# Kernel optimization log

Measured on AMD Instinct MI355X. Metric: run time of the kernel, lower is better.

Reference implementation:

```python
import jax, jax.numpy as jnp
import numpy as np

N = 12000      # nodes
E = 384000     # edges (avg degree 32)
IN, HID, OUT = 128, 128, 40
BETA, ITERS = 0.5, 25   # Bjorck order-2 projection params (module defaults)


def setup_inputs() -> dict:
    key = jax.random.key(0)
    ks = jax.random.split(key, 6)
    x = jax.random.normal(ks[0], (N, IN), jnp.float32)
    edge_index = jax.random.randint(ks[1], (2, E), 0, N, dtype=jnp.int32)
    W1 = jax.random.normal(ks[2], (HID, IN), jnp.float32)
    W2 = jax.random.normal(ks[3], (HID, HID), jnp.float32)
    lin_w = jax.random.normal(ks[4], (OUT, HID), jnp.float32) / np.float32(np.sqrt(HID))
    lin_b = jax.random.normal(ks[5], (OUT,), jnp.float32) * 0.01
    return {"x": x, "W1": W1, "W2": W2, "lin_w": lin_w, "lin_b": lin_b,
            "edge_index": edge_index}


def _bjorck(w):
    # order-2 Bjorck orthonormalization (beta fixed at 0.5):
    # w <- 15/8 w - 5/4 w(w^T w) + 3/8 w(w^T w)^2
    for _ in range(ITERS):
        wtw = w.T @ w
        w = 1.875 * w - 1.25 * (w @ wtw) + 0.375 * (w @ (wtw @ wtw))
    return w


def _orthonormal(W):
    # scale_values: sqrt(||W||_inf * ||W||_1) upper-bounds the spectral norm
    # (computed on .data in torch -> stop_gradient here)
    scaling = jnp.sqrt(jnp.abs(W).sum(axis=1).max() * jnp.abs(W).sum(axis=0).max())
    scaling = jax.lax.stop_gradient(scaling)
    return _bjorck(W.T / scaling).T  # [out, in]


def _normalized_adj(edge_index):
    # to_dense_adj (scatter-add) then D^{-1/2} A^T D^{-1/2} exactly as
    # normalize_tensor_adj: adj.dot(D^{-1/2}).T.dot(D^{-1/2})
    r, c = edge_index[0], edge_index[1]
    adj = jnp.zeros((N, N), jnp.float32).at[r, c].add(1.0)
    rowsum = adj.sum(axis=1)
    d = jnp.where(rowsum > 0, rowsum ** -0.5, 0.0)
    return d[:, None] * adj.T * d[None, :]


def reference(x, W1, W2, lin_w, lin_b, edge_index):
    norm_adj = _normalized_adj(edge_index)          # [N, N]
    h = jax.nn.relu(norm_adj @ (x @ _orthonormal(W1).T))   # [N, HID]
    h = jax.nn.relu(norm_adj @ (h @ _orthonormal(W2).T))   # [N, HID]
    # dropout inactive (eval mode)
    logits = h @ lin_w.T + lin_b                    # [N, OUT]
    return jax.nn.log_softmax(logits, axis=1)
```

## Files before the change

### kernel.cpp

```cpp
#include <hip/hip_runtime.h>
#include <math.h>

#define NN 12000
#define EE 384000
#define FF 128
#define NOUT 40
#define BJ_MAX 25
#define NWARM 8
#define EXIT_TOL 3e-3f
#define GEMM_BLOCKS ((NN + 63) / 64)
#define SEG1 3
#define SEG2 6
#define SEG3 9

typedef __attribute__((ext_vector_type(8))) short bf16x8;
typedef __attribute__((ext_vector_type(4))) short s16x4;
typedef __attribute__((ext_vector_type(4))) float f32x4;
typedef unsigned short ushort_t;

__device__ __forceinline__ ushort_t f2bf(float x) {
  unsigned u = __float_as_uint(x);
  unsigned r = (u + 0x7FFFu + ((u >> 16) & 1u)) >> 16;
  return (ushort_t)r;
}
__device__ __forceinline__ float bf2f(ushort_t h) {
  return __uint_as_float(((unsigned)h) << 16);
}
__device__ __forceinline__ int swz(int r, int c) {
  return ((r << 8) + (c << 1)) ^ ((r & 7) << 4);
}

__device__ __forceinline__ void mm_product(const char* Xh, const char* Xl,
    const char* Yh, const char* Yl, int R0, int C0, int lane, f32x4 (&acc)[2][4]) {
  int rl = lane & 15;
  int kq = (lane >> 4) * 8;
  #pragma unroll
  for (int k0 = 0; k0 < 128; k0 += 32) {
    bf16x8 ah[2], al[2];
    #pragma unroll
    for (int i = 0; i < 2; i++) {
      ah[i] = *(const bf16x8*)(Xh + swz(R0 + i * 16 + rl, k0 + kq));
      al[i] = *(const bf16x8*)(Xl + swz(R0 + i * 16 + rl, k0 + kq));
    }
    #pragma unroll
    for (int j = 0; j < 4; j++) {
      bf16x8 bh = *(const bf16x8*)(Yh + swz(C0 + j * 16 + rl, k0 + kq));
      bf16x8 bl = *(const bf16x8*)(Yl + swz(C0 + j * 16 + rl, k0 + kq));
      #pragma unroll
      for (int i = 0; i < 2; i++) {
        acc[i][j] = __builtin_amdgcn_mfma_f32_16x16x32_bf16(ah[i], bh, acc[i][j], 0, 0, 0);
        acc[i][j] = __builtin_amdgcn_mfma_f32_16x16x32_bf16(ah[i], bl, acc[i][j], 0, 0, 0);
        acc[i][j] = __builtin_amdgcn_mfma_f32_16x16x32_bf16(al[i], bh, acc[i][j], 0, 0, 0);
      }
    }
  }
}

__device__ __forceinline__ void store_C(char* Ch, char* Cl, int R0, int C0,
    int lane, f32x4 (&acc)[2][4]) {
  int cl = lane & 15, rq = (lane >> 4) * 4;
  #pragma unroll
  for (int i = 0; i < 2; i++)
  #pragma unroll
  for (int j = 0; j < 4; j++) {
    int col = C0 + j * 16 + cl;
    int row = R0 + i * 16 + rq;
    s16x4 hv, lv;
    #pragma unroll
    for (int t = 0; t < 4; t++) {
      float x = acc[i][j][t];
      ushort_t h = f2bf(x);
      ushort_t lo = f2bf(x - bf2f(h));
      hv[t] = (short)h; lv[t] = (short)lo;
    }
    *(s16x4*)(Ch + swz(col, row)) = hv;
    *(s16x4*)(Cl + swz(col, row)) = lv;
  }
}

__device__ __forceinline__ void store_CR(char* Ch, char* Cl, char* Rh, char* Rl,
    int R0, int C0, int lane, f32x4 (&acc)[2][4]) {
  int cl = lane & 15, rq = (lane >> 4) * 4;
  #pragma unroll
  for (int i = 0; i < 2; i++)
  #pragma unroll
  for (int j = 0; j < 4; j++) {
    int col = C0 + j * 16 + cl;
    int row = R0 + i * 16 + rq;
    s16x4 hv, lv;
    #pragma unroll
    for (int t = 0; t < 4; t++) {
      float x = acc[i][j][t];
      ushort_t h = f2bf(x);
      ushort_t lo = f2bf(x - bf2f(h));
      hv[t] = (short)h; lv[t] = (short)lo;
    }
    *(s16x4*)(Ch + swz(col, row)) = hv;
    *(s16x4*)(Cl + swz(col, row)) = lv;
    #pragma unroll
    for (int t = 0; t < 4; t++) {
      *(ushort_t*)(Rh + swz(row + t, col)) = (ushort_t)(unsigned short)hv[t];
      *(ushort_t*)(Rl + swz(row + t, col)) = (ushort_t)(unsigned short)lv[t];
    }
  }
}

__device__ void bjorck_segment(int L, int s_it, int e_it, int is_last,
    const float* __restrict__ W1, const float* __restrict__ W2,
    ushort_t* __restrict__ wfc, char* __restrict__ state) {
  __shared__ char lds[131072];
  __shared__ float wmax[8];
  char* P0h = lds;
  char* P0l = lds + 32768;
  char* P1h = lds + 65536;
  char* P1l = lds + 98304;
  const float* Wsrc = (L == 0) ? W1 : W2;
  int tid = threadIdx.x;
  int lane = tid & 63;
  int wv = tid >> 6;
  int R0 = (wv >> 1) * 32;
  int C0 = (wv & 1) * 64;
  char* st = state + L * 131072;

  if (s_it == 0) {
    float* f = (float*)lds;
    if (tid < 256) {
      float s = 0.0f;
      if (tid < 128) {
        for (int j = 0; j < FF; j++) s += fabsf(Wsrc[tid * FF + j]);
      } else {
        int c = tid - 128;
        for (int j = 0; j < FF; j++) s += fabsf(Wsrc[j * FF + c]);
      }
      f[tid] = s;
    }
    __syncthreads();
    if (tid == 0) {
      float rm = 0.0f, cm = 0.0f;
      for (int i = 0; i < 128; i++) { rm = fmaxf(rm, f[i]); cm = fmaxf(cm, f[128 + i]); }
      f[256] = 1.0f / sqrtf(rm * cm);
    }
    __syncthreads();
    float inv_s = f[256];
    __syncthreads();
    int r = tid >> 2, c0 = (tid & 3) * 32;
    #pragma unroll
    for (int mm = 0; mm < 32; mm += 8) {
      bf16x8 hv, lv;
      #pragma unroll
      for (int t = 0; t < 8; t++) {
        float x = Wsrc[r * FF + c0 + mm + t] * inv_s;
        ushort_t h = f2bf(x);
        ushort_t lo = f2bf(x - bf2f(h));
        hv[t] = (short)h; lv[t] = (short)lo;
      }
      *(bf16x8*)(P0h + swz(r, c0 + mm)) = hv;
      *(bf16x8*)(P0l + swz(r, c0 + mm)) = lv;
      #pragma unroll
      for (int t = 0; t < 8; t++) {
        *(ushort_t*)(P1h + swz(c0 + mm + t, r)) = (ushort_t)(unsigned short)hv[t];
        *(ushort_t*)(P1l + swz(c0 + mm + t, r)) = (ushort_t)(unsigned short)lv[t];
      }
    }
    __syncthreads();
  } else {
    int4* dst = (int4*)lds;
    const int4* src = (const int4*)st;
    for (int i = tid; i < 8192; i += 512) dst[i] = src[i];
    __syncthreads();
  }

  int done = 0;
  for (int it = s_it; it < e_it; it++) {
    float ca, cb, cc;
    if (it < NWARM)       { ca = 3.4445f; cb = -4.7750f; cc = 2.0315f; }
    else if (it == NWARM) { ca = 2.1479f; cb = -1.7258f; cc = 0.5645f; }
    else                  { ca = 1.875f;  cb = -1.25f;   cc = 0.375f; }

    f32x4 m_acc[2][4] = {};
    mm_product(P0h, P0l, P0h, P0l, R0, C0, lane, m_acc);

    if (it > NWARM) {
      int cl = lane & 15, rq = (lane >> 4) * 4;
      float lmax = 0.0f;
      #pragma unroll
      for (int i = 0; i < 2; i++)
      #pragma unroll
      for (int j = 0; j < 4; j++)
      #pragma unroll
      for (int t = 0; t < 4; t++) {
        int row = R0 + i * 16 + rq + t;
        int col = C0 + j * 16 + cl;
        float d = m_acc[i][j][t] - ((row == col) ? 1.0f : 0.0f);
        lmax = fmaxf(lmax, fabsf(d));
      }
      #pragma unroll
      for (int off = 32; off; off >>= 1) lmax = fmaxf(lmax, __shfl_xor(lmax, off));
      if (lane == 0) wmax[wv] = lmax;
      __syncthreads();
      float gmax = 0.0f;
      #pragma unroll
      for (int w = 0; w < 8; w++) gmax = fmaxf(gmax, wmax[w]);
      if (gmax < EXIT_TOL) { done = 1; break; }
    } else {
      __syncthreads();
    }
    store_C(P0h, P0l, R0, C0, lane, m_acc);
    __syncthreads();

    f32x4 p_acc[2][4] = {};
    mm_product(P0h, P0l, P0h, P0l, R0, C0, lane, p_acc);
    {
      int cl = lane & 15, rq = (lane >> 4) * 4;
      #pragma unroll
      for (int i = 0; i < 2; i++)
      #pragma unroll
      for (int j = 0; j < 4; j++)
      #pragma unroll
      for (int t = 0; t < 4; t++) {
        int row = R0 + i * 16 + rq + t;
        int col = C0 + j * 16 + cl;
        float pv = cb * m_acc[i][j][t] + cc * p_acc[i][j][t];
        if (row == col) pv += ca;
        p_acc[i][j][t] = pv;
      }
    }
    __syncthreads();
    store_C(P0h, P0l, R0, C0, lane, p_acc);
    __syncthreads();

    f32x4 v_acc[2][4] = {};
    mm_product(P0h, P0l, P1h, P1l, R0, C0, lane, v_acc);
    __syncthreads();
    store_CR(P1h, P1l, P0h, P0l, R0, C0, lane, v_acc);
    __syncthreads();
  }

  if (done || is_last) {
    ushort_t* oh = wfc + L * 32768;
    ushort_t* ol = oh + 16384;
    int r = tid >> 2;
    int q = tid & 3;
    #pragma unroll
    for (int b = 0; b < 4; b++) {
      int c0 = q * 32 + b * 8;
      bf16x8 hv = *(const bf16x8*)(P0h + swz(r, c0));
      bf16x8 lv = *(const bf16x8*)(P0l + swz(r, c0));
      *(bf16x8*)(oh + r * FF + c0) = hv;
      *(bf16x8*)(ol + r * FF + c0) = lv;
    }
  } else {
    const int4* src = (const int4*)lds;
    int4* dst = (int4*)st;
    for (int i = tid; i < 8192; i += 512) dst[i] = src[i];
  }
}

__device__ void scan512(const int* __restrict__ cnt, int* __restrict__ rowstart,
    const float* __restrict__ degf, float* __restrict__ dinv) {
  __shared__ int sums[512];
  int tid = threadIdx.x;
  const int CH = 24;
  int base = tid * CH;
  int local[CH];
  int s = 0;
  #pragma unroll
  for (int m = 0; m < CH; m++) {
    int idx = base + m;
    int v = (idx < NN) ? cnt[idx] : 0;
    local[m] = s;
    s += v;
  }
  sums[tid] = s;
  __syncthreads();
  for (int off = 1; off < 512; off <<= 1) {
    int v = (tid >= off) ? sums[tid - off] : 0;
    __syncthreads();
    sums[tid] += v;
    __syncthreads();
  }
  int excl = (tid > 0) ? sums[tid - 1] : 0;
  #pragma unroll
  for (int m = 0; m < CH; m++) {
    int idx = base + m;
    if (idx < NN) rowstart[idx] = excl + local[m];
  }
  if (tid == 511) rowstart[NN] = sums[511];
  for (int i = tid; i < NN; i += 512) {
    float dv = degf[i];
    dinv[i] = (dv > 0.0f) ? (1.0f / sqrtf(dv)) : 0.0f;
  }
}

__global__ __launch_bounds__(512) void k1_seg_deg(const int* __restrict__ ei,
    float* __restrict__ degf, int* __restrict__ cnt,
    const float* __restrict__ W1, const float* __restrict__ W2,
    ushort_t* __restrict__ wfc, char* __restrict__ state) {
  if (blockIdx.x >= 2) {
    int e = (blockIdx.x - 2) * 512 + threadIdx.x;
    if (e < EE) {
      atomicAdd(&degf[ei[e]], 1.0f);
      atomicAdd(&cnt[ei[EE + e]], 1);
    }
    return;
  }
  bjorck_segment(blockIdx.x, 0, SEG1, 0, W1, W2, wfc, state);
}

__global__ __launch_bounds__(512) void k2_seg_scan(const int* __restrict__ cnt,
    int* __restrict__ rowstart, const float* __restrict__ degf, float* __restrict__ dinv,
    const float* __restrict__ W1, const float* __restrict__ W2,
    ushort_t* __restrict__ wfc, char* __restrict__ state) {
  if (blockIdx.x == 2) { scan512(cnt, rowstart, degf, dinv); return; }
  bjorck_segment(blockIdx.x, SEG1, SEG2, 0, W1, W2, wfc, state);
}

__global__ __launch_bounds__(512) void k3_seg_scatter(const int* __restrict__ ei,
    const int* __restrict__ rowstart, int* __restrict__ fill, int* __restrict__ srcl,
    const float* __restrict__ W1, const float* __restrict__ W2,
    ushort_t* __restrict__ wfc, char* __restrict__ state) {
  if (blockIdx.x >= 2) {
    int e = (blockIdx.x - 2) * 512 + threadIdx.x;
    if (e < EE) {
      int r = ei[e], c = ei[EE + e];
      int pos = rowstart[c] + atomicAdd(&fill[c], 1);
      srcl[pos] = r;
    }
    return;
  }
  bjorck_segment(blockIdx.x, SEG2, SEG3, 0, W1, W2, wfc, state);
}

__global__ __launch_bounds__(512) void k4_seg_spmm(const float* __restrict__ X,
    float* __restrict__ Sout, const float* __restrict__ dinv,
    const int* __restrict__ rowstart, const int* __restrict__ srcl,
    const float* __restrict__ W1, const float* __restrict__ W2,
    ushort_t* __restrict__ wfc, char* __restrict__ state) {
  if (blockIdx.x >= 2) {
    int g = threadIdx.x >> 5, lane32 = threadIdx.x & 31;
    int row = (blockIdx.x - 2) * 16 + g;
    int s = rowstart[row], e = rowstart[row + 1];
    const float4* G4 = (const float4*)X;
    float4 a0 = make_float4(0.f, 0.f, 0.f, 0.f);
    float4 a1 = make_float4(0.f, 0.f, 0.f, 0.f);
    int p = s;
    for (; p + 2 <= e; p += 2) {
      int r0 = srcl[p], r1 = srcl[p + 1];
      float d0 = dinv[r0], d1 = dinv[r1];
      float4 g0 = G4[r0 * 32 + lane32];
      float4 g1 = G4[r1 * 32 + lane32];
      a0.x += d0 * g0.x; a0.y += d0 * g0.y; a0.z += d0 * g0.z; a0.w += d0 * g0.w;
      a1.x += d1 * g1.x; a1.y += d1 * g1.y; a1.z += d1 * g1.z; a1.w += d1 * g1.w;
    }
    if (p < e) {
      int r0 = srcl[p];
      float d0 = dinv[r0];
      float4 g0 = G4[r0 * 32 + lane32];
      a0.x += d0 * g0.x; a0.y += d0 * g0.y; a0.z += d0 * g0.z; a0.w += d0 * g0.w;
    }
    float dc = dinv[row];
    float4 o;
    o.x = dc * (a0.x + a1.x); o.y = dc * (a0.y + a1.y);
    o.z = dc * (a0.z + a1.z); o.w = dc * (a0.w + a1.w);
    ((float4*)Sout)[row * 32 + lane32] = o;
    return;
  }
  bjorck_segment(blockIdx.x, SEG3, BJ_MAX, 1, W1, W2, wfc, state);
}

__global__ __launch_bounds__(256) void gemm_mfma(const float* __restrict__ X,
    const ushort_t* __restrict__ wc, float* __restrict__ Out, int do_relu) {
  __shared__ char xlds[32768];
  char* Xh = xlds;
  char* Xl = xlds + 16384;
  int tid = threadIdx.x;
  int row0 = blockIdx.x * 64;

  {
    int r = tid >> 2;
    int q = (tid & 3) * 32;
    int gr = row0 + r;
    #pragma unroll
    for (int b = 0; b < 32; b += 8) {
      bf16x8 hv, lv;
      if (gr < NN) {
        const float4* xp4 = (const float4*)(X + gr * FF + q + b);
        float4 v0 = xp4[0];
        float4 v1 = xp4[1];
        float xv[8] = {v0.x, v0.y, v0.z, v0.w, v1.x, v1.y, v1.z, v1.w};
        #pragma unroll
        for (int t = 0; t < 8; t++) {
          ushort_t h = f2bf(xv[t]);
          hv[t] = (short)h;
          lv[t] = (short)f2bf(xv[t] - bf2f(h));
        }
      } else {
        #pragma unroll
        for (int t = 0; t < 8; t++) { hv[t] = 0; lv[t] = 0; }
      }
      *(bf16x8*)(Xh + swz(r, q + b)) = hv;
      *(bf16x8*)(Xl + swz(r, q + b)) = lv;
    }
  }
  __syncthreads();

  int lane = tid & 63, wv = tid >> 6;
  int R0 = (wv & 1) * 32;
  int C0 = (wv >> 1) * 64;
  int rl = lane & 15, kq = (lane >> 4) * 8;
  f32x4 acc[2][4] = {};
  #pragma unroll
  for (int k0 = 0; k0 < 128; k0 += 32) {
    bf16x8 ah[2], al[2];
    #pragma unroll
    for (int i = 0; i < 2; i++) {
      ah[i] = *(const bf16x8*)(Xh + swz(R0 + i * 16 + rl, k0 + kq));
      al[i] = *(const bf16x8*)(Xl + swz(R0 + i * 16 + rl, k0 + kq));
    }
    #pragma unroll
    for (int j = 0; j < 4; j++) {
      const ushort_t* bp = wc + (C0 + j * 16 + rl) * FF + k0 + kq;
      bf16x8 bh = *(const bf16x8*)bp;
      bf16x8 bl = *(const bf16x8*)(bp + 16384);
      #pragma unroll
      for (int i = 0; i < 2; i++) {
        acc[i][j] = __builtin_amdgcn_mfma_f32_16x16x32_bf16(ah[i], bh, acc[i][j], 0, 0, 0);
        acc[i][j] = __builtin_amdgcn_mfma_f32_16x16x32_bf16(ah[i], bl, acc[i][j], 0, 0, 0);
        acc[i][j] = __builtin_amdgcn_mfma_f32_16x16x32_bf16(al[i], bh, acc[i][j], 0, 0, 0);
      }
    }
  }
  int rq = (lane >> 4) * 4;
  #pragma unroll
  for (int i = 0; i < 2; i++)
  #pragma unroll
  for (int j = 0; j < 4; j++) {
    int col = C0 + j * 16 + rl;
    #pragma unroll
    for (int t = 0; t < 4; t++) {
      int node = row0 + R0 + i * 16 + rq + t;
      float v = acc[i][j][t];
      if (do_relu) v = fmaxf(v, 0.0f);
      if (node < NN) Out[node * FF + col] = v;
    }
  }
}

__global__ __launch_bounds__(256) void spmm_head(const float* __restrict__ G,
    const float* __restrict__ dinv, const int* __restrict__ rowstart,
    const int* __restrict__ srcl, const float* __restrict__ lw,
    const float* __restrict__ lb, float* __restrict__ out) {
  __shared__ float slw[NOUT * 130];
  __shared__ float slb[64];
  __shared__ float sh[8][128];
  int tid = threadIdx.x;
  for (int i = tid; i < NOUT * 32; i += 256) {
    int r = i >> 5, c4 = i & 31;
    float4 v = ((const float4*)lw)[r * 32 + c4];
    float* dst = slw + r * 130 + c4 * 4;
    dst[0] = v.x; dst[1] = v.y; dst[2] = v.z; dst[3] = v.w;
  }
  if (tid < 64) slb[tid] = (tid < NOUT) ? lb[tid] : 0.0f;

  {
    int g = tid >> 5, lane32 = tid & 31;
    int row = blockIdx.x * 8 + g;
    int s = rowstart[row], e = rowstart[row + 1];
    const float4* G4 = (const float4*)G;
    float4 a0 = make_float4(0.f, 0.f, 0.f, 0.f);
    float4 a1 = make_float4(0.f, 0.f, 0.f, 0.f);
    int p = s;
    for (; p + 2 <= e; p += 2) {
      int r0 = srcl[p], r1 = srcl[p + 1];
      float d0 = dinv[r0], d1 = dinv[r1];
      float4 g0 = G4[r0 * 32 + lane32];
      float4 g1 = G4[r1 * 32 + lane32];
      a0.x += d0 * g0.x; a0.y += d0 * g0.y; a0.z += d0 * g0.z; a0.w += d0 * g0.w;
      a1.x += d1 * g1.x; a1.y += d1 * g1.y; a1.z += d1 * g1.z; a1.w += d1 * g1.w;
    }
    if (p < e) {
      int r0 = srcl[p];
      float d0 = dinv[r0];
      float4 g0 = G4[r0 * 32 + lane32];
      a0.x += d0 * g0.x; a0.y += d0 * g0.y; a0.z += d0 * g0.z; a0.w += d0 * g0.w;
    }
    float dc = dinv[row];
    float4 o;
    o.x = fmaxf(dc * (a0.x + a1.x), 0.f); o.y = fmaxf(dc * (a0.y + a1.y), 0.f);
    o.z = fmaxf(dc * (a0.z + a1.z), 0.f); o.w = fmaxf(dc * (a0.w + a1.w), 0.f);
    ((float4*)&sh[g][0])[lane32] = o;
  }
  __syncthreads();

  int lane = tid & 63, w = tid >> 6;
  int ll = (lane < NOUT) ? lane : 0;
  const float2* wrow = (const float2*)(slw + ll * 130);
  #pragma unroll
  for (int rr = 0; rr < 2; rr++) {
    int lrow = w * 2 + rr;
    int node = blockIdx.x * 8 + lrow;
    const float2* hrow = (const float2*)&sh[lrow][0];
    float val = slb[lane];
    #pragma unroll 4
    for (int k = 0; k < 64; k++) {
      float2 w2 = wrow[k];
      float2 h2 = hrow[k];
      val += w2.x * h2.x + w2.y * h2.y;
    }
    float m = (lane < NOUT) ? val : -INFINITY;
    for (int off = 32; off; off >>= 1) m = fmaxf(m, __shfl_down(m, off));
    m = __shfl(m, 0);
    float ex = (lane < NOUT) ? expf(val - m) : 0.0f;
    float ssum = ex;
    for (int off = 32; off; off >>= 1) ssum += __shfl_down(ssum, off);
    ssum = __shfl(ssum, 0);
    if (lane < NOUT) out[node * NOUT + lane] = val - m - logf(ssum);
  }
}

extern "C" void kernel_launch(void* const* d_in, const int* in_sizes, int n_in,
                              void* d_out, int out_size, void* d_ws, size_t ws_size,
                              hipStream_t stream) {
  const float* x  = (const float*)d_in[0];
  const float* W1 = (const float*)d_in[1];
  const float* W2 = (const float*)d_in[2];
  const float* lw = (const float*)d_in[3];
  const float* lb = (const float*)d_in[4];
  const int*   ei = (const int*)d_in[5];
  float* out = (float*)d_out;

  float* base = (float*)d_ws;
  float* wf   = base;
  float* degf = wf + 32768;
  int* cnt      = (int*)(degf + NN);
  int* fill     = cnt + NN;
  float* dinv = (float*)(fill + NN);
  int* rowstart = (int*)(dinv + NN);
  int* srcl     = rowstart + 12004;
  float* bufA = (float*)(srcl + EE);
  float* bufB = bufA + NN * FF;
  char* state = (char*)(bufB + NN * FF);
  ushort_t* wfc = (ushort_t*)wf;

  (void)hipMemsetAsync(degf, 0, 3 * NN * sizeof(float), stream);

  k1_seg_deg<<<2 + (EE + 511) / 512, 512, 0, stream>>>(ei, degf, cnt, W1, W2, wfc, state);
  k2_seg_scan<<<3, 512, 0, stream>>>(cnt, rowstart, degf, dinv, W1, W2, wfc, state);
  k3_seg_scatter<<<2 + (EE + 511) / 512, 512, 0, stream>>>(ei, rowstart, fill, srcl, W1, W2, wfc, state);
  k4_seg_spmm<<<2 + NN / 16, 512, 0, stream>>>(x, bufA, dinv, rowstart, srcl, W1, W2, wfc, state);

  gemm_mfma<<<GEMM_BLOCKS, 256, 0, stream>>>(bufA, wfc, bufB, 1);
  gemm_mfma<<<GEMM_BLOCKS, 256, 0, stream>>>(bufB, wfc + 32768, bufA, 0);
  spmm_head<<<NN / 8, 256, 0, stream>>>(bufA, dinv, rowstart, srcl, lw, lb, out);
}
```

Baseline: 241.3 us.

## Replace global atomic degree count and CSR scatter with LDS-privatized histograms

Degree and in-count computation now uses 8 blocks that each build a private LDS histogram over a slice of edges and write partial counts, which the scan block sums. The memset goes away. The CSR scatter is split so each of 8 blocks owns a 1500-node destination range and scans all edges, filling it with LDS atomics instead of global atomics. This removes global atomic contention but uses only 8 worker blocks, and each scatter block rereads the whole edge list, so these phases may become serial-latency bound while running alongside the Bjorck blocks. LDS is now declared per kernel and passed into bjorck_segment.

```diff
diff --git a/kernel.cpp b/kernel.cpp
--- a/kernel.cpp
+++ b/kernel.cpp
@@ -12,6 +12,8 @@
 #define SEG1 3
 #define SEG2 6
 #define SEG3 9
+#define NDB 8
+#define DRANGE 1500
 
 typedef __attribute__((ext_vector_type(8))) short bf16x8;
 typedef __attribute__((ext_vector_type(4))) short s16x4;
@@ -105,11 +107,9 @@
   }
 }
 
-__device__ void bjorck_segment(int L, int s_it, int e_it, int is_last,
-    const float* __restrict__ W1, const float* __restrict__ W2,
+__device__ void bjorck_segment(char* lds, float* wmax, int L, int s_it, int e_it,
+    int is_last, const float* __restrict__ W1, const float* __restrict__ W2,
     ushort_t* __restrict__ wfc, char* __restrict__ state) {
-  __shared__ char lds[131072];
-  __shared__ float wmax[8];
   char* P0h = lds;
   char* P0l = lds + 32768;
   char* P1h = lds + 65536;
@@ -256,79 +256,125 @@
   }
 }
 
-__device__ void scan512(const int* __restrict__ cnt, int* __restrict__ rowstart,
-    const float* __restrict__ degf, float* __restrict__ dinv) {
-  __shared__ int sums[512];
-  int tid = threadIdx.x;
-  const int CH = 24;
-  int base = tid * CH;
-  int local[CH];
-  int s = 0;
-  #pragma unroll
-  for (int m = 0; m < CH; m++) {
-    int idx = base + m;
-    int v = (idx < NN) ? cnt[idx] : 0;
-    local[m] = s;
-    s += v;
-  }
-  sums[tid] = s;
-  __syncthreads();
-  for (int off = 1; off < 512; off <<= 1) {
-    int v = (tid >= off) ? sums[tid - off] : 0;
-    __syncthreads();
-    sums[tid] += v;
-    __syncthreads();
-  }
-  int excl = (tid > 0) ? sums[tid - 1] : 0;
-  #pragma unroll
-  for (int m = 0; m < CH; m++) {
-    int idx = base + m;
-    if (idx < NN) rowstart[idx] = excl + local[m];
-  }
-  if (tid == 511) rowstart[NN] = sums[511];
-  for (int i = tid; i < NN; i += 512) {
-    float dv = degf[i];
-    dinv[i] = (dv > 0.0f) ? (1.0f / sqrtf(dv)) : 0.0f;
-  }
-}
-
 __global__ __launch_bounds__(512) void k1_seg_deg(const int* __restrict__ ei,
-    float* __restrict__ degf, int* __restrict__ cnt,
+    int* __restrict__ pr, int* __restrict__ pc,
     const float* __restrict__ W1, const float* __restrict__ W2,
     ushort_t* __restrict__ wfc, char* __restrict__ state) {
+  __shared__ char lds[131072];
+  __shared__ float wmax[8];
   if (blockIdx.x >= 2) {
-    int e = (blockIdx.x - 2) * 512 + threadIdx.x;
-    if (e < EE) {
-      atomicAdd(&degf[ei[e]], 1.0f);
-      atomicAdd(&cnt[ei[EE + e]], 1);
+    int b = blockIdx.x - 2;
+    int* hist = (int*)lds;
+    int tid = threadIdx.x;
+    for (int i = tid; i < 24000; i += 512) hist[i] = 0;
+    __syncthreads();
+    const int4* r4 = (const int4*)ei + b * 12000;
+    const int4* c4 = (const int4*)(ei + EE) + b * 12000;
+    for (int i = tid; i < 12000; i += 512) {
+      int4 rv = r4[i];
+      int4 cv = c4[i];
+      atomicAdd(&hist[rv.x], 1); atomicAdd(&hist[rv.y], 1);
+      atomicAdd(&hist[rv.z], 1); atomicAdd(&hist[rv.w], 1);
+      atomicAdd(&hist[12000 + cv.x], 1); atomicAdd(&hist[12000 + cv.y], 1);
+      atomicAdd(&hist[12000 + cv.z], 1); atomicAdd(&hist[12000 + cv.w], 1);
+    }
+    __syncthreads();
+    int* prb = pr + b * 12000;
+    int* pcb = pc + b * 12000;
+    for (int i = tid; i < 12000; i += 512) {
+      prb[i] = hist[i];
+      pcb[i] = hist[12000 + i];
     }
     return;
   }
-  bjorck_segment(blockIdx.x, 0, SEG1, 0, W1, W2, wfc, state);
-}
-
-__global__ __launch_bounds__(512) void k2_seg_scan(const int* __restrict__ cnt,
-    int* __restrict__ rowstart, const float* __restrict__ degf, float* __restrict__ dinv,
+  bjorck_segment(lds, wmax, blockIdx.x, 0, SEG1, 0, W1, W2, wfc, state);
+}
+
+__global__ __launch_bounds__(512) void k2_seg_scan(const int* __restrict__ pr,
+    const int* __restrict__ pc, int* __restrict__ rowstart, float* __restrict__ dinv,
     const float* __restrict__ W1, const float* __restrict__ W2,
     ushort_t* __restrict__ wfc, char* __restrict__ state) {
-  if (blockIdx.x == 2) { scan512(cnt, rowstart, degf, dinv); return; }
-  bjorck_segment(blockIdx.x, SEG1, SEG2, 0, W1, W2, wfc, state);
+  __shared__ char lds[131072];
+  __shared__ float wmax[8];
+  if (blockIdx.x == 2) {
+    int* sums = (int*)lds;
+    int tid = threadIdx.x;
+    const int CH = 24;
+    int base = tid * CH;
+    int local[CH];
+    int s = 0;
+    #pragma unroll
+    for (int m = 0; m < CH; m++) {
+      int idx = base + m;
+      int v = 0;
+      if (idx < NN) {
+        #pragma unroll
+        for (int b = 0; b < NDB; b++) v += pc[b * 12000 + idx];
+      }
+      local[m] = s;
+      s += v;
+    }
+    sums[tid] = s;
+    __syncthreads();
+    for (int off = 1; off < 512; off <<= 1) {
+      int v = (tid >= off) ? sums[tid - off] : 0;
+      __syncthreads();
+      sums[tid] += v;
+      __syncthreads();
+    }
+    int excl = (tid > 0) ? sums[tid - 1] : 0;
+    #pragma unroll
+    for (int m = 0; m < CH; m++) {
+      int idx = base + m;
+      if (idx < NN) rowstart[idx] = excl + local[m];
+    }
+    if (tid == 511) rowstart[NN] = sums[511];
+    for (int i = tid; i < NN; i += 512) {
+      int dv = 0;
+      #pragma unroll
+      for (int b = 0; b < NDB; b++) dv += pr[b * 12000 + i];
+      dinv[i] = (dv > 0) ? (1.0f / sqrtf((float)dv)) : 0.0f;
+    }
+    return;
+  }
+  bjorck_segment(lds, wmax, blockIdx.x, SEG1, SEG2, 0, W1, W2, wfc, state);
 }
 
 __global__ __launch_bounds__(512) void k3_seg_scatter(const int* __restrict__ ei,
-    const int* __restrict__ rowstart, int* __restrict__ fill, int* __restrict__ srcl,
+    const int* __restrict__ rowstart, int* __restrict__ srcl,
     const float* __restrict__ W1, const float* __restrict__ W2,
     ushort_t* __restrict__ wfc, char* __restrict__ state) {
+  __shared__ char lds[131072];
+  __shared__ float wmax[8];
   if (blockIdx.x >= 2) {
-    int e = (blockIdx.x - 2) * 512 + threadIdx.x;
-    if (e < EE) {
-      int r = ei[e], c = ei[EE + e];
-      int pos = rowstart[c] + atomicAdd(&fill[c], 1);
-      srcl[pos] = r;
+    int b = blockIdx.x - 2;
+    int base = b * DRANGE;
+    int* fillL = (int*)lds;
+    int* rsL = fillL + DRANGE;
+    int tid = threadIdx.x;
+    for (int i = tid; i < DRANGE; i += 512) {
+      fillL[i] = 0;
+      rsL[i] = rowstart[base + i];
+    }
+    __syncthreads();
+    const int4* r4 = (const int4*)ei;
+    const int4* c4 = (const int4*)(ei + EE);
+    for (int i = tid; i < EE / 4; i += 512) {
+      int4 cv = c4[i];
+      int4 rv = r4[i];
+      int d;
+      d = cv.x - base;
+      if ((unsigned)d < (unsigned)DRANGE) srcl[rsL[d] + atomicAdd(&fillL[d], 1)] = rv.x;
+      d = cv.y - base;
+      if ((unsigned)d < (unsigned)DRANGE) srcl[rsL[d] + atomicAdd(&fillL[d], 1)] = rv.y;
+      d = cv.z - base;
+      if ((unsigned)d < (unsigned)DRANGE) srcl[rsL[d] + atomicAdd(&fillL[d], 1)] = rv.z;
+      d = cv.w - base;
+      if ((unsigned)d < (unsigned)DRANGE) srcl[rsL[d] + atomicAdd(&fillL[d], 1)] = rv.w;
     }
     return;
   }
-  bjorck_segment(blockIdx.x, SEG2, SEG3, 0, W1, W2, wfc, state);
+  bjorck_segment(lds, wmax, blockIdx.x, SEG2, SEG3, 0, W1, W2, wfc, state);
 }
 
 __global__ __launch_bounds__(512) void k4_seg_spmm(const float* __restrict__ X,
@@ -336,6 +382,8 @@
     const int* __restrict__ rowstart, const int* __restrict__ srcl,
     const float* __restrict__ W1, const float* __restrict__ W2,
     ushort_t* __restrict__ wfc, char* __restrict__ state) {
+  __shared__ char lds[131072];
+  __shared__ float wmax[8];
   if (blockIdx.x >= 2) {
     int g = threadIdx.x >> 5, lane32 = threadIdx.x & 31;
     int row = (blockIdx.x - 2) * 16 + g;
@@ -365,7 +413,7 @@
     ((float4*)Sout)[row * 32 + lane32] = o;
     return;
   }
-  bjorck_segment(blockIdx.x, SEG3, BJ_MAX, 1, W1, W2, wfc, state);
+  bjorck_segment(lds, wmax, blockIdx.x, SEG3, BJ_MAX, 1, W1, W2, wfc, state);
 }
 
 __global__ __launch_bounds__(256) void gemm_mfma(const float* __restrict__ X,
@@ -531,10 +579,9 @@
 
   float* base = (float*)d_ws;
   float* wf   = base;
-  float* degf = wf + 32768;
-  int* cnt      = (int*)(degf + NN);
-  int* fill     = cnt + NN;
-  float* dinv = (float*)(fill + NN);
+  int* pr     = (int*)(wf + 32768);
+  int* pc     = pr + NDB * 12000;
+  float* dinv = (float*)(pc + NDB * 12000);
   int* rowstart = (int*)(dinv + NN);
   int* srcl     = rowstart + 12004;
   float* bufA = (float*)(srcl + EE);
@@ -542,11 +589,9 @@
   char* state = (char*)(bufB + NN * FF);
   ushort_t* wfc = (ushort_t*)wf;
 
-  (void)hipMemsetAsync(degf, 0, 3 * NN * sizeof(float), stream);
-
-  k1_seg_deg<<<2 + (EE + 511) / 512, 512, 0, stream>>>(ei, degf, cnt, W1, W2, wfc, state);
-  k2_seg_scan<<<3, 512, 0, stream>>>(cnt, rowstart, degf, dinv, W1, W2, wfc, state);
-  k3_seg_scatter<<<2 + (EE + 511) / 512, 512, 0, stream>>>(ei, rowstart, fill, srcl, W1, W2, wfc, state);
+  k1_seg_deg<<<2 + NDB, 512, 0, stream>>>(ei, pr, pc, W1, W2, wfc, state);
+  k2_seg_scan<<<3, 512, 0, stream>>>(pr, pc, rowstart, dinv, W1, W2, wfc, state);
+  k3_seg_scatter<<<2 + NDB, 512, 0, stream>>>(ei, rowstart, srcl, W1, W2, wfc, state);
   k4_seg_spmm<<<2 + NN / 16, 512, 0, stream>>>(x, bufA, dinv, rowstart, srcl, W1, W2, wfc, state);
 
   gemm_mfma<<<GEMM_BLOCKS, 256, 0, stream>>>(bufA, wfc, bufB, 1);
```

After: 383.1 us. 58.7% more time.
